# Performance work log

Measured on AMD Instinct MI355X. Metric: run time of the kernel, lower is better.

Reference implementation:

```python
import jax, jax.numpy as jnp
import numpy as np

EMB_DIM = 256
NUM_RELATIONS = 128
BATCH = 4096
LOG_SQRT_2PI = 0.9189385332046727  # 0.5*log(2*pi)


def setup_inputs() -> dict:
    key = jax.random.key(0)
    k1, k2, k3, k4, k5 = jax.random.split(key, 5)
    sbjs = jax.random.normal(k1, (BATCH, EMB_DIM), dtype=jnp.float32)
    objs = jax.random.normal(k2, (BATCH, EMB_DIM), dtype=jnp.float32)
    mus = jax.random.normal(k3, (NUM_RELATIONS, 2 * EMB_DIM), dtype=jnp.float32)
    sigmas = jnp.abs(jax.random.normal(k4, (NUM_RELATIONS, 2 * EMB_DIM), dtype=jnp.float32)) + 1.0
    relation_priors = jax.random.normal(k5, (NUM_RELATIONS,), dtype=jnp.float32)
    return {"sbjs": sbjs, "objs": objs, "mus": mus, "sigmas": sigmas,
            "relation_priors": relation_priors}


def reference(sbjs, objs, mus, sigmas, relation_priors):
    # x: [B, 2D] concatenated subject/object embeddings
    x = jnp.concatenate([sbjs, objs], axis=1)
    two_d = x.shape[1]
    # Gaussian log-pdf, broadcast over relations: [B, R, 2D]
    z = (x[:, None, :] - mus[None, :, :]) / sigmas[None, :, :]
    logp = -0.5 * z * z - jnp.log(sigmas)[None, :, :] - LOG_SQRT_2PI
    # Original adds prior to every one of the 2D dims before the sum,
    # so the prior contributes prior * 2D to each [b, r] output.
    return logp.sum(axis=-1) + relation_priors[None, :] * two_d
```

## Files before the change

kernel.cpp:

```cpp
#include <hip/hip_runtime.h>
#include <hip/hip_bf16.h>
#include <cstddef>
#include <cstdint>

#define EMB   256
#define TWOD  512
#define NREL  128
#define BATCH 4096
#define LOG_SQRT_2PI 0.9189385332046727f

typedef __bf16 bf16x8 __attribute__((ext_vector_type(8)));
typedef float  f32x4  __attribute__((ext_vector_type(4)));

__device__ __forceinline__ unsigned short f2bf(float f) {
    unsigned u = __builtin_bit_cast(unsigned, f);
    u = (u + 0x7FFFu + ((u >> 16) & 1u)) >> 16;
    return (unsigned short)u;
}

__global__ __launch_bounds__(256) void nb_prep(
    const float* __restrict__ mus, const float* __restrict__ sigmas,
    const float* __restrict__ priors,
    unsigned short* __restrict__ Wc, unsigned short* __restrict__ Wa,
    float* __restrict__ cst)
{
    const int r = blockIdx.x;
    const int tid = threadIdx.x;
    float esum = 0.0f;
    #pragma unroll
    for (int i = 0; i < 2; i++) {
        const int k = tid + i * 256;
        const float mu = mus[r * TWOD + k];
        const float s  = sigmas[r * TWOD + k];
        const float inv2 = 1.0f / (s * s);
        const float a = -0.5f * inv2;
        const float c = mu * inv2;
        esum += -0.5f * mu * mu * inv2 - logf(s) - LOG_SQRT_2PI;
        const int idx = (k >> 3) * (NREL * 8) + r * 8 + (k & 7);
        Wc[idx] = f2bf(c);
        Wa[idx] = f2bf(a);
    }
    __shared__ float red[4];
    #pragma unroll
    for (int off = 32; off >= 1; off >>= 1)
        esum += __shfl_down(esum, off, 64);
    if ((tid & 63) == 0) red[tid >> 6] = esum;
    __syncthreads();
    if (tid == 0)
        cst[r] = red[0] + red[1] + red[2] + red[3] + priors[r] * (float)TWOD;
}

#define BGM 64
#define KSPLIT 8
#define PART_STRIDE ((size_t)BATCH * NREL)

__device__ __forceinline__ void gl_lds16(const void* g, void* l) {
    __builtin_amdgcn_global_load_lds(
        (const __attribute__((address_space(1))) unsigned int*)g,
        (__attribute__((address_space(3))) unsigned int*)l, 16, 0, 0);
}

__global__ __launch_bounds__(256) void nb_gemm(
    const float* __restrict__ sbjs, const float* __restrict__ objs,
    const unsigned short* __restrict__ Wc, const unsigned short* __restrict__ Wa,
    const float* __restrict__ cst, float* __restrict__ dst, int use_atomic)
{
    __shared__ __align__(16) unsigned short sYx [8 * 520];
    __shared__ __align__(16) unsigned short sYx2[8 * 520];
    __shared__ __align__(16) unsigned short sWc [8 * NREL * 8];
    __shared__ __align__(16) unsigned short sWa [8 * NREL * 8];

    const int tid  = threadIdx.x;
    const int wv   = tid >> 6;
    const int lane = tid & 63;
    const int m16  = lane & 15;
    const int quad = lane >> 4;
    const int b0   = blockIdx.x * BGM;
    const int kb   = blockIdx.y;
    const int k0   = kb * 64;

    const unsigned short* wcg = Wc + (size_t)kb * 8 * NREL * 8;
    const unsigned short* wag = Wa + (size_t)kb * 8 * NREL * 8;
    #pragma unroll
    for (int c = 0; c < 4; c++) {
        const int off = (wv * 4 + c) * 512 + lane * 8;
        gl_lds16(wcg + off, &sWc[off]);
        gl_lds16(wag + off, &sWa[off]);
    }

    const float* xb = (k0 < EMB) ? (sbjs + k0) : (objs + (k0 - EMB));
    #pragma unroll
    for (int i = 0; i < 4; i++) {
        const int idx = tid + i * 256;
        const int m   = idx >> 4;
        const int c4  = idx & 15;
        const float4 v = *(const float4*)(xb + (size_t)(b0 + m) * EMB + c4 * 4);
        ushort4 px = { f2bf(v.x), f2bf(v.y), f2bf(v.z), f2bf(v.w) };
        ushort4 p2 = { f2bf(v.x * v.x), f2bf(v.y * v.y),
                       f2bf(v.z * v.z), f2bf(v.w * v.w) };
        const int yoff = (c4 >> 1) * 520 + m * 8 + (c4 & 1) * 4;
        *(ushort4*)(&sYx [yoff]) = px;
        *(ushort4*)(&sYx2[yoff]) = p2;
    }
    __syncthreads();

    f32x4 acc[4][2];
    #pragma unroll
    for (int mt = 0; mt < 4; mt++)
        #pragma unroll
        for (int nt = 0; nt < 2; nt++) acc[mt][nt] = (f32x4)0.0f;

    #pragma unroll
    for (int ks = 0; ks < 2; ks++) {
        const int k8 = ks * 4 + quad;
        bf16x8 ax[4], ax2[4], bc[2], ba[2];
        #pragma unroll
        for (int mt = 0; mt < 4; mt++) {
            const int o = k8 * 520 + (mt * 16 + m16) * 8;
            ax [mt] = *(const bf16x8*)(&sYx [o]);
            ax2[mt] = *(const bf16x8*)(&sYx2[o]);
        }
        #pragma unroll
        for (int nt = 0; nt < 2; nt++) {
            const int r = wv * 32 + nt * 16 + m16;
            const int o = k8 * (NREL * 8) + r * 8;
            bc[nt] = *(const bf16x8*)(&sWc[o]);
            ba[nt] = *(const bf16x8*)(&sWa[o]);
        }
        #pragma unroll
        for (int mt = 0; mt < 4; mt++)
            #pragma unroll
            for (int nt = 0; nt < 2; nt++) {
                acc[mt][nt] = __builtin_amdgcn_mfma_f32_16x16x32_bf16(
                                  ax [mt], bc[nt], acc[mt][nt], 0, 0, 0);
                acc[mt][nt] = __builtin_amdgcn_mfma_f32_16x16x32_bf16(
                                  ax2[mt], ba[nt], acc[mt][nt], 0, 0, 0);
            }
    }

    if (use_atomic) {
        float* out = dst;
        #pragma unroll
        for (int mt = 0; mt < 4; mt++)
            #pragma unroll
            for (int nt = 0; nt < 2; nt++) {
                const int rr   = wv * 32 + nt * 16 + m16;
                const int brow = b0 + mt * 16 + quad * 4;
                const float ca = (kb == 0) ? cst[rr] : 0.0f;
                #pragma unroll
                for (int reg = 0; reg < 4; reg++)
                    unsafeAtomicAdd(out + (size_t)(brow + reg) * NREL + rr,
                                    acc[mt][nt][reg] + ca);
            }
    } else {
        float* pd = dst + (size_t)kb * PART_STRIDE;
        #pragma unroll
        for (int mt = 0; mt < 4; mt++)
            #pragma unroll
            for (int nt = 0; nt < 2; nt++) {
                const int rr   = wv * 32 + nt * 16 + m16;
                const int brow = b0 + mt * 16 + quad * 4;
                #pragma unroll
                for (int reg = 0; reg < 4; reg++)
                    pd[(size_t)(brow + reg) * NREL + rr] = acc[mt][nt][reg];
            }
    }
}

__global__ __launch_bounds__(256) void nb_reduce(
    const float* __restrict__ partial, const float* __restrict__ cst,
    float* __restrict__ out)
{
    const int idx4 = blockIdx.x * 256 + threadIdx.x;
    const float4* p4 = (const float4*)partial;
    float4 s = p4[idx4];
    #pragma unroll
    for (int kb = 1; kb < KSPLIT; kb++) {
        const float4 v = p4[(size_t)kb * (PART_STRIDE / 4) + idx4];
        s.x += v.x; s.y += v.y; s.z += v.z; s.w += v.w;
    }
    const float4 cv = ((const float4*)cst)[idx4 & 31];
    s.x += cv.x; s.y += cv.y; s.z += cv.z; s.w += cv.w;
    ((float4*)out)[idx4] = s;
}

__global__ __launch_bounds__(256) void nb_slow(
    const float* __restrict__ sbjs, const float* __restrict__ objs,
    const float* __restrict__ mus, const float* __restrict__ sigmas,
    const float* __restrict__ priors, float* __restrict__ out)
{
    const int idx = blockIdx.x * 256 + threadIdx.x;
    const int b = idx >> 7;
    const int r = idx & (NREL - 1);
    float acc = priors[r] * (float)TWOD;
    for (int k = 0; k < TWOD; k++) {
        const float x  = (k < EMB) ? sbjs[(size_t)b * EMB + k]
                                   : objs[(size_t)b * EMB + (k - EMB)];
        const float mu = mus[r * TWOD + k];
        const float s  = sigmas[r * TWOD + k];
        const float z  = (x - mu) / s;
        acc += -0.5f * z * z - logf(s) - LOG_SQRT_2PI;
    }
    out[idx] = acc;
}

extern "C" void kernel_launch(void* const* d_in, const int* in_sizes, int n_in,
                              void* d_out, int out_size, void* d_ws, size_t ws_size,
                              hipStream_t stream)
{
    const float* sbjs   = (const float*)d_in[0];
    const float* objs   = (const float*)d_in[1];
    const float* mus    = (const float*)d_in[2];
    const float* sigmas = (const float*)d_in[3];
    const float* priors = (const float*)d_in[4];
    float* out = (float*)d_out;

    char* ws = (char*)d_ws;
    const size_t o_wc  = 0;
    const size_t o_wa  = 128 << 10;
    const size_t o_cst = 256 << 10;
    const size_t o_par = (256 << 10) + 4096;
    const size_t need_par = o_par + (size_t)KSPLIT * PART_STRIDE * sizeof(float);
    const size_t need_at  = o_par;

    if (ws_size >= need_at) {
        unsigned short* Wc = (unsigned short*)(ws + o_wc);
        unsigned short* Wa = (unsigned short*)(ws + o_wa);
        float* cst = (float*)(ws + o_cst);
        nb_prep<<<NREL, 256, 0, stream>>>(mus, sigmas, priors, Wc, Wa, cst);
        if (ws_size >= need_par) {
            float* partial = (float*)(ws + o_par);
            nb_gemm<<<dim3(BATCH / BGM, KSPLIT), 256, 0, stream>>>(
                sbjs, objs, Wc, Wa, cst, partial, 0);
            nb_reduce<<<(BATCH * NREL / 4) / 256, 256, 0, stream>>>(partial, cst, out);
        } else {
            hipMemsetAsync(out, 0, (size_t)BATCH * NREL * sizeof(float), stream);
            nb_gemm<<<dim3(BATCH / BGM, KSPLIT), 256, 0, stream>>>(
                sbjs, objs, Wc, Wa, cst, out, 1);
        }
    } else {
        nb_slow<<<(BATCH * NREL) / 256, 256, 0, stream>>>(
            sbjs, objs, mus, sigmas, priors, out);
    }
}
```

Baseline: 80.34 us.

## Replace split-K GEMM and reduce with fused full-K kernel using double-buffered weights

Removes the split-K partial buffer and the separate reduction kernel. Each block now handles 16 batch rows across the full 512-wide K dimension. Activations and their squares are held in registers as bf16, and weight chunks are streamed into LDS with double-buffered async global-to-LDS loads. The constant term is added in the epilogue. This removes the partial write/read round trip and one launch, but every block re-streams the full 256KB weight set and the grid holds only 256 blocks at one block per SM.

```diff
diff --git a/kernel.cpp b/kernel.cpp
--- a/kernel.cpp
+++ b/kernel.cpp
@@ -9,13 +9,27 @@
 #define BATCH 4096
 #define LOG_SQRT_2PI 0.9189385332046727f
 
-typedef __bf16 bf16x8 __attribute__((ext_vector_type(8)));
-typedef float  f32x4  __attribute__((ext_vector_type(4)));
+typedef __bf16          bf16x8  __attribute__((ext_vector_type(8)));
+typedef unsigned short  u16x8   __attribute__((ext_vector_type(8)));
+typedef float           f32x4   __attribute__((ext_vector_type(4)));
 
 __device__ __forceinline__ unsigned short f2bf(float f) {
     unsigned u = __builtin_bit_cast(unsigned, f);
     u = (u + 0x7FFFu + ((u >> 16) & 1u)) >> 16;
     return (unsigned short)u;
+}
+
+__device__ __forceinline__ bf16x8 pack8(float4 a, float4 b) {
+    u16x8 u;
+    u[0] = f2bf(a.x); u[1] = f2bf(a.y); u[2] = f2bf(a.z); u[3] = f2bf(a.w);
+    u[4] = f2bf(b.x); u[5] = f2bf(b.y); u[6] = f2bf(b.z); u[7] = f2bf(b.w);
+    return __builtin_bit_cast(bf16x8, u);
+}
+
+__device__ __forceinline__ void gl_lds16(const void* g, void* l) {
+    __builtin_amdgcn_global_load_lds(
+        (const __attribute__((address_space(1))) unsigned int*)g,
+        (__attribute__((address_space(3))) unsigned int*)l, 16, 0, 0);
 }
 
 __global__ __launch_bounds__(256) void nb_prep(
@@ -33,12 +47,10 @@
         const float mu = mus[r * TWOD + k];
         const float s  = sigmas[r * TWOD + k];
         const float inv2 = 1.0f / (s * s);
-        const float a = -0.5f * inv2;
-        const float c = mu * inv2;
         esum += -0.5f * mu * mu * inv2 - logf(s) - LOG_SQRT_2PI;
         const int idx = (k >> 3) * (NREL * 8) + r * 8 + (k & 7);
-        Wc[idx] = f2bf(c);
-        Wa[idx] = f2bf(a);
+        Wc[idx] = f2bf(mu * inv2);
+        Wa[idx] = f2bf(-0.5f * inv2);
     }
     __shared__ float red[4];
     #pragma unroll
@@ -50,138 +62,100 @@
         cst[r] = red[0] + red[1] + red[2] + red[3] + priors[r] * (float)TWOD;
 }
 
-#define BGM 64
-#define KSPLIT 8
-#define PART_STRIDE ((size_t)BATCH * NREL)
-
-__device__ __forceinline__ void gl_lds16(const void* g, void* l) {
-    __builtin_amdgcn_global_load_lds(
-        (const __attribute__((address_space(1))) unsigned int*)g,
-        (__attribute__((address_space(3))) unsigned int*)l, 16, 0, 0);
-}
-
-__global__ __launch_bounds__(256) void nb_gemm(
+#define CHP  8
+#define NCHK 8
+
+__device__ __forceinline__ void issue_chunk(
+    unsigned short* sW, const unsigned short* Wc, const unsigned short* Wa,
+    int wv, int lane, int ch, int buf)
+{
+    const int t = wv & 1;
+    const unsigned short* g = t ? Wa : Wc;
+    const int pbase = (wv >> 1) * 4;
+    #pragma unroll
+    for (int j = 0; j < 4; j++) {
+        #pragma unroll
+        for (int h = 0; h < 2; h++) {
+            const int p    = pbase + j;
+            const int goff = (ch * CHP + p) * 1024 + h * 512 + lane * 8;
+            const int loff = buf * 16384 + t * 8192 + p * 1024 + h * 512;
+            gl_lds16(g + goff, &sW[loff]);
+        }
+    }
+}
+
+__global__ __launch_bounds__(256, 1) void nb_fused(
     const float* __restrict__ sbjs, const float* __restrict__ objs,
     const unsigned short* __restrict__ Wc, const unsigned short* __restrict__ Wa,
-    const float* __restrict__ cst, float* __restrict__ dst, int use_atomic)
-{
-    __shared__ __align__(16) unsigned short sYx [8 * 520];
-    __shared__ __align__(16) unsigned short sYx2[8 * 520];
-    __shared__ __align__(16) unsigned short sWc [8 * NREL * 8];
-    __shared__ __align__(16) unsigned short sWa [8 * NREL * 8];
+    const float* __restrict__ cst, float* __restrict__ out)
+{
+    __shared__ unsigned short sW[2 * 2 * CHP * 1024];
 
     const int tid  = threadIdx.x;
     const int wv   = tid >> 6;
     const int lane = tid & 63;
     const int m16  = lane & 15;
     const int quad = lane >> 4;
-    const int b0   = blockIdx.x * BGM;
-    const int kb   = blockIdx.y;
-    const int k0   = kb * 64;
-
-    const unsigned short* wcg = Wc + (size_t)kb * 8 * NREL * 8;
-    const unsigned short* wag = Wa + (size_t)kb * 8 * NREL * 8;
-    #pragma unroll
-    for (int c = 0; c < 4; c++) {
-        const int off = (wv * 4 + c) * 512 + lane * 8;
-        gl_lds16(wcg + off, &sWc[off]);
-        gl_lds16(wag + off, &sWa[off]);
-    }
-
-    const float* xb = (k0 < EMB) ? (sbjs + k0) : (objs + (k0 - EMB));
-    #pragma unroll
-    for (int i = 0; i < 4; i++) {
-        const int idx = tid + i * 256;
-        const int m   = idx >> 4;
-        const int c4  = idx & 15;
-        const float4 v = *(const float4*)(xb + (size_t)(b0 + m) * EMB + c4 * 4);
-        ushort4 px = { f2bf(v.x), f2bf(v.y), f2bf(v.z), f2bf(v.w) };
-        ushort4 p2 = { f2bf(v.x * v.x), f2bf(v.y * v.y),
-                       f2bf(v.z * v.z), f2bf(v.w * v.w) };
-        const int yoff = (c4 >> 1) * 520 + m * 8 + (c4 & 1) * 4;
-        *(ushort4*)(&sYx [yoff]) = px;
-        *(ushort4*)(&sYx2[yoff]) = p2;
-    }
+    const int b0   = blockIdx.x * 16;
+
+    issue_chunk(sW, Wc, Wa, wv, lane, 0, 0);
+
+    bf16x8 ax[16], ax2[16];
+    {
+        const int row = b0 + m16;
+        #pragma unroll
+        for (int fi = 0; fi < 16; fi++) {
+            const int col = fi * 32 + quad * 8;
+            const float* p = (col < EMB)
+                ? (sbjs + (size_t)row * EMB + col)
+                : (objs + (size_t)row * EMB + (col - EMB));
+            const float4 v0 = *(const float4*)p;
+            const float4 v1 = *(const float4*)(p + 4);
+            ax[fi] = pack8(v0, v1);
+            const float4 s0 = {v0.x * v0.x, v0.y * v0.y, v0.z * v0.z, v0.w * v0.w};
+            const float4 s1 = {v1.x * v1.x, v1.y * v1.y, v1.z * v1.z, v1.w * v1.w};
+            ax2[fi] = pack8(s0, s1);
+        }
+    }
+
+    f32x4 acc[2];
+    acc[0] = (f32x4)0.0f;
+    acc[1] = (f32x4)0.0f;
+
     __syncthreads();
 
-    f32x4 acc[4][2];
-    #pragma unroll
-    for (int mt = 0; mt < 4; mt++)
-        #pragma unroll
-        for (int nt = 0; nt < 2; nt++) acc[mt][nt] = (f32x4)0.0f;
-
-    #pragma unroll
-    for (int ks = 0; ks < 2; ks++) {
-        const int k8 = ks * 4 + quad;
-        bf16x8 ax[4], ax2[4], bc[2], ba[2];
-        #pragma unroll
-        for (int mt = 0; mt < 4; mt++) {
-            const int o = k8 * 520 + (mt * 16 + m16) * 8;
-            ax [mt] = *(const bf16x8*)(&sYx [o]);
-            ax2[mt] = *(const bf16x8*)(&sYx2[o]);
-        }
-        #pragma unroll
-        for (int nt = 0; nt < 2; nt++) {
-            const int r = wv * 32 + nt * 16 + m16;
-            const int o = k8 * (NREL * 8) + r * 8;
-            bc[nt] = *(const bf16x8*)(&sWc[o]);
-            ba[nt] = *(const bf16x8*)(&sWa[o]);
-        }
-        #pragma unroll
-        for (int mt = 0; mt < 4; mt++)
+    #pragma unroll
+    for (int ch = 0; ch < NCHK; ch++) {
+        const int buf = ch & 1;
+        if (ch + 1 < NCHK)
+            issue_chunk(sW, Wc, Wa, wv, lane, ch + 1, buf ^ 1);
+
+        #pragma unroll
+        for (int ks2 = 0; ks2 < 2; ks2++) {
+            const int fi = ch * 2 + ks2;
+            const int pb = buf * 16384 + (ks2 * 4 + quad) * 1024;
             #pragma unroll
             for (int nt = 0; nt < 2; nt++) {
-                acc[mt][nt] = __builtin_amdgcn_mfma_f32_16x16x32_bf16(
-                                  ax [mt], bc[nt], acc[mt][nt], 0, 0, 0);
-                acc[mt][nt] = __builtin_amdgcn_mfma_f32_16x16x32_bf16(
-                                  ax2[mt], ba[nt], acc[mt][nt], 0, 0, 0);
+                const int r  = wv * 32 + nt * 16 + m16;
+                const bf16x8 bc = *(const bf16x8*)&sW[pb + r * 8];
+                const bf16x8 ba = *(const bf16x8*)&sW[pb + 8192 + r * 8];
+                acc[nt] = __builtin_amdgcn_mfma_f32_16x16x32_bf16(
+                              ax[fi],  bc, acc[nt], 0, 0, 0);
+                acc[nt] = __builtin_amdgcn_mfma_f32_16x16x32_bf16(
+                              ax2[fi], ba, acc[nt], 0, 0, 0);
             }
-    }
-
-    if (use_atomic) {
-        float* out = dst;
-        #pragma unroll
-        for (int mt = 0; mt < 4; mt++)
-            #pragma unroll
-            for (int nt = 0; nt < 2; nt++) {
-                const int rr   = wv * 32 + nt * 16 + m16;
-                const int brow = b0 + mt * 16 + quad * 4;
-                const float ca = (kb == 0) ? cst[rr] : 0.0f;
-                #pragma unroll
-                for (int reg = 0; reg < 4; reg++)
-                    unsafeAtomicAdd(out + (size_t)(brow + reg) * NREL + rr,
-                                    acc[mt][nt][reg] + ca);
-            }
-    } else {
-        float* pd = dst + (size_t)kb * PART_STRIDE;
-        #pragma unroll
-        for (int mt = 0; mt < 4; mt++)
-            #pragma unroll
-            for (int nt = 0; nt < 2; nt++) {
-                const int rr   = wv * 32 + nt * 16 + m16;
-                const int brow = b0 + mt * 16 + quad * 4;
-                #pragma unroll
-                for (int reg = 0; reg < 4; reg++)
-                    pd[(size_t)(brow + reg) * NREL + rr] = acc[mt][nt][reg];
-            }
-    }
-}
-
-__global__ __launch_bounds__(256) void nb_reduce(
-    const float* __restrict__ partial, const float* __restrict__ cst,
-    float* __restrict__ out)
-{
-    const int idx4 = blockIdx.x * 256 + threadIdx.x;
-    const float4* p4 = (const float4*)partial;
-    float4 s = p4[idx4];
-    #pragma unroll
-    for (int kb = 1; kb < KSPLIT; kb++) {
-        const float4 v = p4[(size_t)kb * (PART_STRIDE / 4) + idx4];
-        s.x += v.x; s.y += v.y; s.z += v.z; s.w += v.w;
-    }
-    const float4 cv = ((const float4*)cst)[idx4 & 31];
-    s.x += cv.x; s.y += cv.y; s.z += cv.z; s.w += cv.w;
-    ((float4*)out)[idx4] = s;
+        }
+        __syncthreads();
+    }
+
+    #pragma unroll
+    for (int nt = 0; nt < 2; nt++) {
+        const int r = wv * 32 + nt * 16 + m16;
+        const float ca = cst[r];
+        #pragma unroll
+        for (int reg = 0; reg < 4; reg++)
+            out[(size_t)(b0 + quad * 4 + reg) * NREL + r] = acc[nt][reg] + ca;
+    }
 }
 
 __global__ __launch_bounds__(256) void nb_slow(
@@ -217,27 +191,16 @@
 
     char* ws = (char*)d_ws;
     const size_t o_wc  = 0;
-    const size_t o_wa  = 128 << 10;
-    const size_t o_cst = 256 << 10;
-    const size_t o_par = (256 << 10) + 4096;
-    const size_t need_par = o_par + (size_t)KSPLIT * PART_STRIDE * sizeof(float);
-    const size_t need_at  = o_par;
-
-    if (ws_size >= need_at) {
-        unsigned short* Wc = (unsigned short*)(ws + o_wc);
-        unsigned short* Wa = (unsigned short*)(ws + o_wa);
+    const size_t o_wa  = 256 << 10;
+    const size_t o_cst = 512 << 10;
+    const size_t need  = o_cst + NREL * sizeof(float);
+
+    if (ws_size >= need) {
+        unsigned short* Wcp = (unsigned short*)(ws + o_wc);
+        unsigned short* Wap = (unsigned short*)(ws + o_wa);
         float* cst = (float*)(ws + o_cst);
-        nb_prep<<<NREL, 256, 0, stream>>>(mus, sigmas, priors, Wc, Wa, cst);
-        if (ws_size >= need_par) {
-            float* partial = (float*)(ws + o_par);
-            nb_gemm<<<dim3(BATCH / BGM, KSPLIT), 256, 0, stream>>>(
-                sbjs, objs, Wc, Wa, cst, partial, 0);
-            nb_reduce<<<(BATCH * NREL / 4) / 256, 256, 0, stream>>>(partial, cst, out);
-        } else {
-            hipMemsetAsync(out, 0, (size_t)BATCH * NREL * sizeof(float), stream);
-            nb_gemm<<<dim3(BATCH / BGM, KSPLIT), 256, 0, stream>>>(
-                sbjs, objs, Wc, Wa, cst, out, 1);
-        }
+        nb_prep<<<NREL, 256, 0, stream>>>(mus, sigmas, priors, Wcp, Wap, cst);
+        nb_fused<<<BATCH / 16, 256, 0, stream>>>(sbjs, objs, Wcp, Wap, cst, out);
     } else {
         nb_slow<<<(BATCH * NREL) / 256, 256, 0, stream>>>(
             sbjs, objs, mus, sigmas, priors, out);
```

Result: faster. 73.47 us (-8.5%).
